# Kernel optimization log

Hardware: AMD Instinct MI355X
Metric: run time of the kernel (lower is better)

The kernel has to match this reference:

```python
import jax, jax.numpy as jnp
import numpy as np

N_HEADS = 16
D_K = 64
MAX_REL = 32


def setup_inputs() -> dict:
    key = jax.random.key(0)
    k1, k2, k3, k4 = jax.random.split(key, 4)
    B, T, D = 2, 2048, 1024
    x = jax.random.normal(k1, (B, T, D), dtype=jnp.float32)
    # torch nn.Linear weights are [out, in]; y = x @ W.T
    W_q = jax.random.normal(k2, (D, D), dtype=jnp.float32) / np.sqrt(D)
    W_o = jax.random.normal(k3, (D, D), dtype=jnp.float32) / np.sqrt(D)
    rel_k_emb = jax.random.normal(k4, (2 * MAX_REL + 1, D_K), dtype=jnp.float32)
    return {"x": x, "W_q": W_q, "W_o": W_o, "rel_k_emb": rel_k_emb}


def reference(x, W_q, W_o, rel_k_emb):
    B, T, D = x.shape
    H, dk = N_HEADS, D_K
    scale = 1.0 / np.sqrt(dk).astype(np.float32)
    # NOTE: source module (faithfully) uses W_q for q, k AND v.
    q = (x @ W_q.T).reshape(B, T, H, dk).transpose(0, 2, 1, 3)  # [B,H,T,dk]
    k = q
    v = q
    scores = jnp.einsum('bhid,bhjd->bhij', q, k) * scale  # [B,H,T,T]
    pos = jnp.arange(T)
    rel = jnp.clip(pos[:, None] - pos[None, :], -MAX_REL, MAX_REL) + MAX_REL  # [T,T]
    rel_keys = rel_k_emb[rel]  # [T,T,dk]
    rel_logits = jnp.einsum('bhid,ijd->bhij', q, rel_keys) * scale
    scores = scores + rel_logits
    attn = jax.nn.softmax(scores, axis=-1)
    out = jnp.einsum('bhij,bhjd->bhid', attn, v)  # [B,H,T,dk]
    out = out.transpose(0, 2, 1, 3).reshape(B, T, D)
    return out @ W_o.T
```

## Files before the change

### kernel.cpp

```cpp
#include <hip/hip_runtime.h>
#include <stdint.h>

typedef unsigned short u16;
typedef __attribute__((ext_vector_type(8))) short short8;
typedef __attribute__((ext_vector_type(4))) float f32x4;

#define MFMA16(a, b, c) __builtin_amdgcn_mfma_f32_16x16x32_bf16((a), (b), (c), 0, 0, 0)

__device__ __forceinline__ void gload16(const void* g, void* l) {
  __builtin_amdgcn_global_load_lds((const __attribute__((address_space(1))) void*)g,
                                   (__attribute__((address_space(3))) void*)l, 16, 0, 0);
}

__device__ __forceinline__ u16 bf16bits(float f) {
  union { float f; unsigned u; } x; x.f = f;
  unsigned r = x.u + 0x7fffu + ((x.u >> 16) & 1u);
  return (u16)(r >> 16);
}

__device__ __forceinline__ float bf16tof(u16 b) {
  union { unsigned u; float f; } x; x.u = ((unsigned)b) << 16;
  return x.f;
}

__device__ __forceinline__ float exp2fast(float x) {
  float r;
  asm("v_exp_f32 %0, %1" : "=v"(r) : "v"(x));
  return r;
}

__global__ __launch_bounds__(256) void cvt4(const float* __restrict__ s0, u16* __restrict__ d0, int n0,
                                            const float* __restrict__ s1, u16* __restrict__ d1, int n1,
                                            const float* __restrict__ s2, u16* __restrict__ d2, int n2,
                                            const float* __restrict__ s3, u16* __restrict__ d3, int n3) {
  const float* s; u16* d; int n;
  switch (blockIdx.y) {
    case 0:  s = s0; d = d0; n = n0; break;
    case 1:  s = s1; d = d1; n = n1; break;
    case 2:  s = s2; d = d2; n = n2; break;
    default: s = s3; d = d3; n = n3; break;
  }
  int stride = gridDim.x * blockDim.x;
  for (int i = blockIdx.x * blockDim.x + threadIdx.x; i * 8 < n; i += stride) {
    float4 a = ((const float4*)s)[i * 2];
    float4 b = ((const float4*)s)[i * 2 + 1];
    union { u16 u[8]; uint4 v; } pk;
    pk.u[0] = bf16bits(a.x); pk.u[1] = bf16bits(a.y);
    pk.u[2] = bf16bits(a.z); pk.u[3] = bf16bits(a.w);
    pk.u[4] = bf16bits(b.x); pk.u[5] = bf16bits(b.y);
    pk.u[6] = bf16bits(b.z); pk.u[7] = bf16bits(b.w);
    ((uint4*)d)[i] = pk.v;
  }
}

template <int EPI>
__global__ __launch_bounds__(256) void gemm_bt(const u16* __restrict__ A,
                                               const u16* __restrict__ Bw,
                                               u16* __restrict__ out0,
                                               u16* __restrict__ out1,
                                               float* __restrict__ outf,
                                               int M, int N, int K) {
  __shared__ __align__(16) char smem[2 * 12288];
  const int tid = threadIdx.x;
  const int lane = tid & 63, w = tid >> 6;
  const int g = lane >> 4, l15 = lane & 15;
  const int m0 = blockIdx.y * 128, n0 = blockIdx.x * 64;
  const int wm = w >> 1, wn = w & 1;
  const int NK = K >> 5;
  f32x4 acc[4][2] = {};

  auto stage = [&](int kk, int buf) {
    char* Ab_l = smem + buf * 12288;
    char* Bb_l = smem + buf * 12288 + 8192;
    const char* Ab = (const char*)A + ((size_t)m0 * K + kk * 32) * 2;
#pragma unroll
    for (int i = 0; i < 2; ++i) {
      int rowblk = w + 4 * i;
      int row = rowblk * 16 + (lane >> 2);
      gload16(Ab + (size_t)row * (K * 2) + (lane & 3) * 16, Ab_l + rowblk * 1024);
    }
    const char* Bb = (const char*)Bw + ((size_t)n0 * K + kk * 32) * 2;
    int rowb = w * 16 + (lane >> 2);
    gload16(Bb + (size_t)rowb * (K * 2) + (lane & 3) * 16, Bb_l + w * 1024);
  };

  stage(0, 0);
  __syncthreads();
  for (int kk = 0; kk < NK; ++kk) {
    int buf = kk & 1;
    if (kk + 1 < NK) stage(kk + 1, buf ^ 1);
    const char* Abuf = smem + buf * 12288;
    const char* Bbuf = Abuf + 8192;
    short8 af[4], bfr[2];
#pragma unroll
    for (int mt = 0; mt < 4; ++mt)
      af[mt] = *(const short8*)(Abuf + (wm * 64 + mt * 16 + l15) * 64 + g * 16);
#pragma unroll
    for (int nt = 0; nt < 2; ++nt)
      bfr[nt] = *(const short8*)(Bbuf + (wn * 32 + nt * 16 + l15) * 64 + g * 16);
#pragma unroll
    for (int mt = 0; mt < 4; ++mt)
#pragma unroll
      for (int nt = 0; nt < 2; ++nt)
        acc[mt][nt] = MFMA16(af[mt], bfr[nt], acc[mt][nt]);
    __syncthreads();
  }

#pragma unroll
  for (int mt = 0; mt < 4; ++mt)
#pragma unroll
    for (int nt = 0; nt < 2; ++nt) {
      int n = n0 + wn * 32 + nt * 16 + l15;
      int mbase = m0 + wm * 64 + mt * 16 + 4 * g;
      if constexpr (EPI == 0) {
#pragma unroll
        for (int r = 0; r < 4; ++r)
          outf[(size_t)(mbase + r) * N + n] = acc[mt][nt][r];
      } else {
        int b = mbase >> 11, t = mbase & 2047;
        int h = n >> 6, d = n & 63;
        size_t bhb = (size_t)(b * 16 + h) * (2048 * 64);
        union { u16 u[4]; uint2 v; } pk;
#pragma unroll
        for (int r = 0; r < 4; ++r) {
          u16 uu = bf16bits(acc[mt][nt][r]);
          out0[bhb + (size_t)(t + r) * 64 + d] = uu;
          pk.u[r] = uu;
        }
        *(uint2*)(out1 + bhb + (size_t)d * 2048 + t) = pk.v;
      }
    }
}

__global__ __launch_bounds__(256) void attn_rel(const u16* __restrict__ qtd,
                                                const u16* __restrict__ qdt,
                                                const u16* __restrict__ relk,
                                                u16* __restrict__ outa) {
  __shared__ __align__(16) char smem[49664];
  const int tid = threadIdx.x;
  const int lane = tid & 63, w = tid >> 6;
  const int g = lane >> 4, l15 = lane & 15;
  int lin = blockIdx.y * 32 + blockIdx.x;
  int sidx = lin >> 3;
  const int bh = (lin & 7) * 4 + (sidx & 3);
  const int q0 = (sidx >> 2) * 64;
  const int q0w = q0 + w * 16;
  u16* qrelb = (u16*)(smem + 32768);
  char* Pbuf = smem + 41472 + w * 2048;

  short8 qa[2];
  {
    size_t rowoff = ((size_t)bh * 2048 + q0w + l15) * 64;
    qa[0] = *(const short8*)(qtd + rowoff + g * 8);
    qa[1] = *(const short8*)(qtd + rowoff + g * 8 + 32);
    const float QS = 0.18033688f;
#pragma unroll
    for (int c = 0; c < 2; ++c)
#pragma unroll
      for (int e = 0; e < 8; ++e)
        qa[c][e] = (short)bf16bits(bf16tof((u16)qa[c][e]) * QS);
  }

  for (int c = tid; c < 520; c += 256)
    *(uint4*)(smem + c * 16) = *(const uint4*)((const char*)relk + c * 16);
  for (int c = 520 + tid; c < 640; c += 256) {
    uint4 z; z.x = 0u; z.y = 0u; z.z = 0u; z.w = 0u;
    *(uint4*)(smem + c * 16) = z;
  }
  __syncthreads();

  f32x4 aq[5] = {};
#pragma unroll
  for (int t = 0; t < 5; ++t)
#pragma unroll
    for (int c = 0; c < 2; ++c) {
      short8 rb = *(const short8*)(smem + ((t * 16 + l15) * 64 + g * 8 + c * 32) * 2);
      aq[t] = MFMA16(qa[c], rb, aq[t]);
    }
  float qlo[4], qhi[4];
#pragma unroll
  for (int r = 0; r < 4; ++r) {
    qlo[r] = __shfl(aq[0][r], lane & 48);
    qhi[r] = __shfl(aq[4][r], lane & 48);
  }
#pragma unroll
  for (int t = 0; t < 5; ++t)
    if (t < 4 || l15 == 0)
#pragma unroll
      for (int r = 0; r < 4; ++r)
        qrelb[(w * 16 + 4 * g + r) * 68 + t * 16 + l15] = bf16bits(aq[t][r]);
  __syncthreads();

  auto stageKV = [&](int kv0, int buf) {
    char* Kb = smem + buf * 16384;
    char* Vb = Kb + 8192;
    int sub = lane >> 3, chunk = lane & 7;
#pragma unroll
    for (int i = 0; i < 2; ++i) {
      int rloc = (w * 2 + i) * 8 + sub;
      int swz = (chunk * 16) ^ ((rloc & 7) << 4);
      gload16((const char*)qtd + ((size_t)bh * 2048 + kv0 + rloc) * 128 + swz,
              Kb + (w * 2 + i) * 1024);
      gload16((const char*)qdt + ((size_t)bh * 64 + rloc) * 4096 + kv0 * 2 + swz,
              Vb + (w * 2 + i) * 1024);
    }
  };

  f32x4 aco[4] = {};
  f32x4 accl = {};
  short8 ones;
  {
    short ov = (l15 == 0) ? (short)0x3F80 : (short)0;
#pragma unroll
    for (int e = 0; e < 8; ++e) ones[e] = ov;
  }

  stageKV(0, 0);
  __syncthreads();
  for (int ti = 0; ti < 32; ++ti) {
    int buf = ti & 1;
    int kv0 = ti * 64;
    if (ti + 1 < 32) stageKV(kv0 + 64, buf ^ 1);
    const char* Kb = smem + buf * 16384;
    const char* Vb = Kb + 8192;

    f32x4 s[4];
    bool farL = (q0w - (kv0 + 63)) >= 32;
    bool farR = (q0w + 15 - kv0) <= -32;
    if (farL) {
      f32x4 b;
#pragma unroll
      for (int r = 0; r < 4; ++r) b[r] = qhi[r];
#pragma unroll
      for (int jt = 0; jt < 4; ++jt) s[jt] = b;
    } else if (farR) {
      f32x4 b;
#pragma unroll
      for (int r = 0; r < 4; ++r) b[r] = qlo[r];
#pragma unroll
      for (int jt = 0; jt < 4; ++jt) s[jt] = b;
    } else {
#pragma unroll
      for (int jt = 0; jt < 4; ++jt) {
        int jg = kv0 + jt * 16 + l15;
#pragma unroll
        for (int r = 0; r < 4; ++r) {
          int dd = (q0w + 4 * g + r) - jg;
          dd = dd < -32 ? -32 : (dd > 32 ? 32 : dd);
          s[jt][r] = bf16tof(qrelb[(w * 16 + 4 * g + r) * 68 + dd + 32]);
        }
      }
    }

#pragma unroll
    for (int jt = 0; jt < 4; ++jt) {
      int jloc = jt * 16 + l15;
      int sw = (jloc & 7) << 4;
#pragma unroll
      for (int c = 0; c < 2; ++c) {
        short8 kb = *(const short8*)(Kb + ((jloc * 128 + g * 16 + c * 64) ^ sw));
        s[jt] = MFMA16(qa[c], kb, s[jt]);
      }
    }

#pragma unroll
    for (int r = 0; r < 4; ++r) {
      int i16 = 4 * g + r;
      int sw = (i16 & 7) << 4;
#pragma unroll
      for (int jt = 0; jt < 4; ++jt) {
        float p = exp2fast(s[jt][r]);
        union { float f; unsigned u; } cv; cv.f = p;
        *(u16*)(Pbuf + ((i16 * 128 + (jt * 16 + l15) * 2) ^ sw)) = (u16)(cv.u >> 16);
      }
    }

    short8 pa[2];
    {
      int sw = (l15 & 7) << 4;
      pa[0] = *(const short8*)(Pbuf + ((l15 * 128 + g * 16) ^ sw));
      pa[1] = *(const short8*)(Pbuf + ((l15 * 128 + g * 16 + 64) ^ sw));
    }
#pragma unroll
    for (int dt = 0; dt < 4; ++dt) {
      int dloc = dt * 16 + l15;
      int sw = (dloc & 7) << 4;
#pragma unroll
      for (int c = 0; c < 2; ++c) {
        short8 vb = *(const short8*)(Vb + ((dloc * 128 + g * 16 + c * 64) ^ sw));
        aco[dt] = MFMA16(pa[c], vb, aco[dt]);
      }
    }
    accl = MFMA16(pa[0], ones, accl);
    accl = MFMA16(pa[1], ones, accl);
    __syncthreads();
  }

  int b = bh >> 4, h = bh & 15;
#pragma unroll
  for (int r = 0; r < 4; ++r) {
    float lr = __shfl(accl[r], lane & 48);
    float rl = 1.0f / lr;
    int t = q0w + 4 * g + r;
    size_t base = ((size_t)(b * 2048 + t) * 16 + h) * 64;
#pragma unroll
    for (int dt = 0; dt < 4; ++dt)
      outa[base + dt * 16 + l15] = bf16bits(aco[dt][r] * rl);
  }
}

extern "C" void kernel_launch(void* const* d_in, const int* in_sizes, int n_in,
                              void* d_out, int out_size, void* d_ws, size_t ws_size,
                              hipStream_t stream) {
  const float* x    = (const float*)d_in[0];
  const float* Wq   = (const float*)d_in[1];
  const float* Wo   = (const float*)d_in[2];
  const float* relk = (const float*)d_in[3];
  float* out = (float*)d_out;

  u16* q_td   = (u16*)d_ws;
  u16* q_dt   = q_td + 4194304;
  u16* x_bf   = q_dt + 4194304;
  u16* wq_bf  = x_bf + 4194304;
  u16* wo_bf  = wq_bf + 1048576;
  u16* rel_bf = wo_bf + 1048576;
  u16* attn   = x_bf;

  cvt4<<<dim3(2048, 4), 256, 0, stream>>>(x, x_bf, 4194304,
                                          Wq, wq_bf, 1048576,
                                          Wo, wo_bf, 1048576,
                                          relk, rel_bf, 4160);
  gemm_bt<1><<<dim3(16, 32), 256, 0, stream>>>(x_bf, wq_bf, q_td, q_dt, nullptr,
                                               4096, 1024, 1024);
  attn_rel<<<dim3(32, 32), 256, 0, stream>>>(q_td, q_dt, rel_bf, attn);
  gemm_bt<0><<<dim3(16, 32), 256, 0, stream>>>(attn, wo_bf, nullptr, nullptr, out,
                                               4096, 1024, 1024);
}
```

Baseline: 119.4 us.

## Transpose score MFMA so P is written in packed rows and row sums computed in registers

The score MFMAs swap operand order so each lane holds a column of query rows across four consecutive keys. This lets exp'd probabilities be packed into 8-byte stores to the P buffer instead of scalar 2-byte stores. Row sums are accumulated in registers and reduced with cross-lane shuffles, which replaces the two extra MFMAs against a ones vector. The relative-bias table is relaid out with a 64-wide stride, which reduces LDS usage, and the far-right clamp value is read from a register. The cost is more index arithmetic in the near-diagonal bias path and extra shuffles at the end.

New measurement: 119.1 us. About the same (-0.2%).

```diff
diff --git a/kernel.cpp b/kernel.cpp
--- a/kernel.cpp
+++ b/kernel.cpp
@@ -136,7 +136,7 @@
                                                 const u16* __restrict__ qdt,
                                                 const u16* __restrict__ relk,
                                                 u16* __restrict__ outa) {
-  __shared__ __align__(16) char smem[49664];
+  __shared__ __align__(16) char smem[49152];
   const int tid = threadIdx.x;
   const int lane = tid & 63, w = tid >> 6;
   const int g = lane >> 4, l15 = lane & 15;
@@ -146,7 +146,7 @@
   const int q0 = (sidx >> 2) * 64;
   const int q0w = q0 + w * 16;
   u16* qrelb = (u16*)(smem + 32768);
-  char* Pbuf = smem + 41472 + w * 2048;
+  char* Pbuf = smem + 40960 + w * 2048;
 
   short8 qa[2];
   {
@@ -175,20 +175,15 @@
 #pragma unroll
     for (int c = 0; c < 2; ++c) {
       short8 rb = *(const short8*)(smem + ((t * 16 + l15) * 64 + g * 8 + c * 32) * 2);
-      aq[t] = MFMA16(qa[c], rb, aq[t]);
-    }
-  float qlo[4], qhi[4];
-#pragma unroll
-  for (int r = 0; r < 4; ++r) {
-    qlo[r] = __shfl(aq[0][r], lane & 48);
-    qhi[r] = __shfl(aq[4][r], lane & 48);
-  }
-#pragma unroll
-  for (int t = 0; t < 5; ++t)
-    if (t < 4 || l15 == 0)
-#pragma unroll
-      for (int r = 0; r < 4; ++r)
-        qrelb[(w * 16 + 4 * g + r) * 68 + t * 16 + l15] = bf16bits(aq[t][r]);
+      aq[t] = MFMA16(rb, qa[c], aq[t]);
+    }
+  float bhi = __shfl(aq[4][0], l15);
+  float blo = __shfl(aq[0][0], l15);
+#pragma unroll
+  for (int t = 0; t < 4; ++t)
+#pragma unroll
+    for (int r = 0; r < 4; ++r)
+      qrelb[(w * 16 + l15) * 64 + t * 16 + 4 * g + r] = bf16bits(aq[t][r]);
   __syncthreads();
 
   auto stageKV = [&](int kv0, int buf) {
@@ -207,13 +202,7 @@
   };
 
   f32x4 aco[4] = {};
-  f32x4 accl = {};
-  short8 ones;
-  {
-    short ov = (l15 == 0) ? (short)0x3F80 : (short)0;
-#pragma unroll
-    for (int e = 0; e < 8; ++e) ones[e] = ov;
-  }
+  float lrow = 0.f;
 
   stageKV(0, 0);
   __syncthreads();
@@ -227,29 +216,21 @@
     f32x4 s[4];
     bool farL = (q0w - (kv0 + 63)) >= 32;
     bool farR = (q0w + 15 - kv0) <= -32;
-    if (farL) {
-      f32x4 b;
-#pragma unroll
-      for (int r = 0; r < 4; ++r) b[r] = qhi[r];
-#pragma unroll
-      for (int jt = 0; jt < 4; ++jt) s[jt] = b;
-    } else if (farR) {
-      f32x4 b;
-#pragma unroll
-      for (int r = 0; r < 4; ++r) b[r] = qlo[r];
-#pragma unroll
-      for (int jt = 0; jt < 4; ++jt) s[jt] = b;
+    if (farL || farR) {
+      float bv = farL ? bhi : blo;
+      f32x4 binit = {bv, bv, bv, bv};
+#pragma unroll
+      for (int jt = 0; jt < 4; ++jt) s[jt] = binit;
     } else {
 #pragma unroll
-      for (int jt = 0; jt < 4; ++jt) {
-        int jg = kv0 + jt * 16 + l15;
+      for (int jt = 0; jt < 4; ++jt)
 #pragma unroll
         for (int r = 0; r < 4; ++r) {
-          int dd = (q0w + 4 * g + r) - jg;
-          dd = dd < -32 ? -32 : (dd > 32 ? 32 : dd);
-          s[jt][r] = bf16tof(qrelb[(w * 16 + 4 * g + r) * 68 + dd + 32]);
+          int dd = (q0w + l15) - (kv0 + jt * 16 + 4 * g + r);
+          int idx = dd < -32 ? 0 : (dd > 31 ? 63 : dd + 32);
+          float tb = bf16tof(qrelb[(w * 16 + l15) * 64 + idx]);
+          s[jt][r] = dd >= 32 ? bhi : tb;
         }
-      }
     }
 
 #pragma unroll
@@ -259,47 +240,49 @@
 #pragma unroll
       for (int c = 0; c < 2; ++c) {
         short8 kb = *(const short8*)(Kb + ((jloc * 128 + g * 16 + c * 64) ^ sw));
-        s[jt] = MFMA16(qa[c], kb, s[jt]);
+        s[jt] = MFMA16(kb, qa[c], s[jt]);
       }
     }
 
-#pragma unroll
-    for (int r = 0; r < 4; ++r) {
-      int i16 = 4 * g + r;
-      int sw = (i16 & 7) << 4;
-#pragma unroll
-      for (int jt = 0; jt < 4; ++jt) {
-        float p = exp2fast(s[jt][r]);
-        union { float f; unsigned u; } cv; cv.f = p;
-        *(u16*)(Pbuf + ((i16 * 128 + (jt * 16 + l15) * 2) ^ sw)) = (u16)(cv.u >> 16);
-      }
-    }
-
-    short8 pa[2];
-    {
-      int sw = (l15 & 7) << 4;
-      pa[0] = *(const short8*)(Pbuf + ((l15 * 128 + g * 16) ^ sw));
-      pa[1] = *(const short8*)(Pbuf + ((l15 * 128 + g * 16 + 64) ^ sw));
-    }
+    float lsum = 0.f;
+    int psw = (l15 & 7) << 4;
+#pragma unroll
+    for (int jt = 0; jt < 4; ++jt) {
+      float p0 = exp2fast(s[jt][0]);
+      float p1 = exp2fast(s[jt][1]);
+      float p2 = exp2fast(s[jt][2]);
+      float p3 = exp2fast(s[jt][3]);
+      lsum += (p0 + p1) + (p2 + p3);
+      union { float f; unsigned u; } c0, c1, c2, c3;
+      c0.f = p0; c1.f = p1; c2.f = p2; c3.f = p3;
+      uint2 wv;
+      wv.x = (c0.u >> 16) | (c1.u & 0xFFFF0000u);
+      wv.y = (c2.u >> 16) | (c3.u & 0xFFFF0000u);
+      *(uint2*)(Pbuf + ((l15 * 128 + jt * 32 + g * 8) ^ psw)) = wv;
+    }
+    lrow += lsum;
+
+    short8 pa0 = *(const short8*)(Pbuf + ((l15 * 128 + g * 16) ^ psw));
+    short8 pa1 = *(const short8*)(Pbuf + ((l15 * 128 + g * 16 + 64) ^ psw));
 #pragma unroll
     for (int dt = 0; dt < 4; ++dt) {
       int dloc = dt * 16 + l15;
       int sw = (dloc & 7) << 4;
-#pragma unroll
-      for (int c = 0; c < 2; ++c) {
-        short8 vb = *(const short8*)(Vb + ((dloc * 128 + g * 16 + c * 64) ^ sw));
-        aco[dt] = MFMA16(pa[c], vb, aco[dt]);
-      }
-    }
-    accl = MFMA16(pa[0], ones, accl);
-    accl = MFMA16(pa[1], ones, accl);
+      short8 vb0 = *(const short8*)(Vb + ((dloc * 128 + g * 16) ^ sw));
+      short8 vb1 = *(const short8*)(Vb + ((dloc * 128 + g * 16 + 64) ^ sw));
+      aco[dt] = MFMA16(pa0, vb0, aco[dt]);
+      aco[dt] = MFMA16(pa1, vb1, aco[dt]);
+    }
     __syncthreads();
   }
 
+  lrow += __shfl_xor(lrow, 16);
+  lrow += __shfl_xor(lrow, 32);
+
   int b = bh >> 4, h = bh & 15;
 #pragma unroll
   for (int r = 0; r < 4; ++r) {
-    float lr = __shfl(accl[r], lane & 48);
+    float lr = __shfl(lrow, 4 * g + r);
     float rl = 1.0f / lr;
     int t = q0w + 4 * g + r;
     size_t base = ((size_t)(b * 2048 + t) * 16 + h) * 64;
```
